# Kernel optimization log

Hardware: AMD Instinct MI355X
Metric: run time of the kernel (lower is better)

The kernel has to match this reference:

```python
import jax, jax.numpy as jnp
import numpy as np

B, Cin, H, W = 8, 128, 64, 64
Cout, K, S, P = 128, 3, 1, 1
KK = K * K


def _conv(x, w, b=None):
    y = jax.lax.conv_general_dilated(
        x, w, window_strides=(S, S), padding=[(P, P), (P, P)],
        dimension_numbers=("NCHW", "OIHW", "NCHW"))
    if b is not None:
        y = y + b[None, :, None, None]
    return y


def setup_inputs() -> dict:
    key = jax.random.key(0)
    ks = jax.random.split(key, 6)
    x = jax.random.normal(ks[0], (B, Cin, H, W), jnp.float32)
    # offset/modulator convs are zero-init in the module; use small random
    # values so learned-offset sampling path is actually exercised.
    w_off = jax.random.normal(ks[1], (2 * KK, Cin, K, K), jnp.float32) * 0.01
    b_off = jax.random.normal(ks[2], (2 * KK,), jnp.float32) * 0.1
    w_mod = jax.random.normal(ks[3], (KK, Cin, K, K), jnp.float32) * 0.01
    b_mod = jax.random.normal(ks[4], (KK,), jnp.float32) * 0.1
    w_reg = jax.random.normal(ks[5], (Cout, Cin, K, K), jnp.float32) * (1.0 / np.sqrt(Cin * KK))
    return {"x": x, "w_off": w_off, "b_off": b_off,
            "w_mod": w_mod, "b_mod": b_mod, "w_reg": w_reg}


def _deform_conv2d(x, offset, mask, w_reg):
    # offset: [B, 2*KK, Hout, Wout] with (dy, dx) interleaved per tap (torchvision layout)
    Hout, Wout = offset.shape[2], offset.shape[3]
    off = offset.reshape(B, KK, 2, Hout, Wout)
    dy = off[:, :, 0].transpose(0, 2, 3, 1)  # [B,Hout,Wout,KK]
    dx = off[:, :, 1].transpose(0, 2, 3, 1)
    kh = (jnp.arange(KK) // K).astype(jnp.float32)
    kw = (jnp.arange(KK) % K).astype(jnp.float32)
    ho = jnp.arange(Hout, dtype=jnp.float32) * S - P
    wo = jnp.arange(Wout, dtype=jnp.float32) * S - P
    py = ho[None, :, None, None] + kh[None, None, None, :] + dy  # [B,Hout,Wout,KK]
    px = wo[None, None, :, None] + kw[None, None, None, :] + dx
    y0f = jnp.floor(py); x0f = jnp.floor(px)
    wy = (py - y0f)[..., None]; wx = (px - x0f)[..., None]
    y0 = y0f.astype(jnp.int32); x0 = x0f.astype(jnp.int32)
    x_bhwc = x.transpose(0, 2, 3, 1)  # [B,H,W,Cin]
    bidx = jnp.arange(B).reshape(B, 1, 1, 1)

    def gather(yi, xi):
        valid = ((yi >= 0) & (yi < H) & (xi >= 0) & (xi < W)).astype(x.dtype)
        v = x_bhwc[bidx, jnp.clip(yi, 0, H - 1), jnp.clip(xi, 0, W - 1)]
        return v * valid[..., None]  # [B,Hout,Wout,KK,Cin], zero outside

    v00 = gather(y0, x0)
    v01 = gather(y0, x0 + 1)
    v10 = gather(y0 + 1, x0)
    v11 = gather(y0 + 1, x0 + 1)
    val = (v00 * (1 - wy) * (1 - wx) + v01 * (1 - wy) * wx
           + v10 * wy * (1 - wx) + v11 * wy * wx)
    # modulated deformable conv v2: mask [B,KK,Hout,Wout]
    val = val * mask.transpose(0, 2, 3, 1)[..., None]
    # weighted accumulation over taps and input channels -> NCHW output
    return jnp.einsum("bhwkc,ock->bohw", val, w_reg.reshape(Cout, Cin, KK))


def reference(x, w_off, b_off, w_mod, b_mod, w_reg):
    offset = _conv(x, w_off, b_off)
    mask = 2.0 * jax.nn.sigmoid(_conv(x, w_mod, b_mod))
    return _deform_conv2d(x, offset, mask, w_reg)
```

## Files before the change

### kernel.cpp

```cpp
#include <hip/hip_runtime.h>
#include <hip/hip_bf16.h>
#include <math.h>

#define H 64
#define W 64
#define CIN 128
#define COUT 128
#define BATCH 8
#define NPIX (H*W)
#define PXT 32
#define AP  136
#define RP  36
#define VSZ (PXT*AP)

typedef __attribute__((ext_vector_type(8))) short bf16x8;
typedef __attribute__((ext_vector_type(4))) float f32x4;
typedef __attribute__((ext_vector_type(16))) float f32x16;

static __device__ inline short f2bf(float f) {
  union { float f; unsigned u; } v; v.f = f;
  unsigned r = v.u + 0x7FFF + ((v.u >> 16) & 1);
  return (short)(r >> 16);
}
static __device__ inline float bf_lo(unsigned u) {
  union { unsigned u; float f; } v; v.u = u << 16; return v.f;
}
static __device__ inline float bf_hi(unsigned u) {
  union { unsigned u; float f; } v; v.u = u & 0xffff0000u; return v.f;
}

__global__ __launch_bounds__(256) void k_prep(const float* __restrict__ x,
    short* __restrict__ xbh,
    const float* __restrict__ w_off, const float* __restrict__ w_mod,
    short* __restrict__ wOMs, const float* __restrict__ w_reg,
    short* __restrict__ wAs) {
  __shared__ float tile[32][65];
  int blk = blockIdx.x;
  int t = threadIdx.x;
  if (blk < 2048) {
    int cg = blk & 3, y = (blk >> 2) & 63, b = blk >> 8;
#pragma unroll
    for (int j = 0; j < 2; ++j) {
      int f = t + j * 256;
      int ci = f >> 4, xi4 = f & 15;
      float4 v = *(const float4*)&x[(((b * CIN + cg * 32 + ci) * H + y) * W) + xi4 * 4];
      *(float4*)&tile[ci][xi4 * 4] = v;
    }
    __syncthreads();
#pragma unroll
    for (int i = 0; i < 2; ++i) {
      int idx = t + i * 256;
      int xi = idx >> 3, cig = idx & 7;
      float f0 = tile[cig * 4 + 0][xi];
      float f1 = tile[cig * 4 + 1][xi];
      float f2 = tile[cig * 4 + 2][xi];
      float f3 = tile[cig * 4 + 3][xi];
      __hip_bfloat162 h01 = __float22bfloat162_rn(make_float2(f0, f1));
      __hip_bfloat162 h23 = __float22bfloat162_rn(make_float2(f2, f3));
      uint2 pk;
      pk.x = *(unsigned*)&h01; pk.y = *(unsigned*)&h23;
      *(uint2*)&xbh[((b * H + y) * W + xi) * CIN + cg * 32 + cig * 4] = pk;
    }
  } else if (blk < 2048 + 144) {
    int e = (blk - 2048) * 256 + t;
    int tap = e >> 12, oc = (e >> 7) & 31, c = e & 127;
    float v = 0.f;
    if (oc < 18)      v = w_off[(oc * 128 + c) * 9 + tap];
    else if (oc < 27) v = w_mod[((oc - 18) * 128 + c) * 9 + tap];
    int kstep = c >> 4, g = (c >> 3) & 1, j = c & 7;
    int lane = g * 32 + oc;
    int o = ((tap * 8 + kstep) * 64 + lane) * 8 + j;
    wOMs[o] = f2bf(v);
  } else {
    int e = (blk - 2192) * 256 + t;
    int tap = e >> 14, oc = (e >> 7) & 127, c = e & 127;
    int kstep = c >> 4, g = (c >> 3) & 1, j = c & 7;
    int ms = oc >> 5, m = oc & 31;
    int lane = g * 32 + m;
    int o = (((tap * 8 + kstep) * 4 + ms) * 64 + lane) * 8 + j;
    wAs[o] = f2bf(w_reg[(oc * 128 + c) * 9 + tap]);
  }
}

__global__ __launch_bounds__(512, 8) void k_deform(const short* __restrict__ xbh,
    const short* __restrict__ wOMs, const float* __restrict__ b_off,
    const float* __restrict__ b_mod, const short* __restrict__ wAs,
    float* __restrict__ out) {
  __shared__ __align__(16) char smem_u[31104];
  __shared__ __align__(16) float  pw[PXT * 9 * 4];
  __shared__ __align__(16) ushort pa4[PXT * 9 * 4];
  float* red  = (float*)smem_u;
  short* vs   = (short*)smem_u;
  float* redE = (float*)smem_u;

  int blk = blockIdx.x;
  int b = blk & 7, tile = blk >> 3;
  int pix0 = tile * PXT;
  int t = threadIdx.x;
  int lane = t & 63;
  int wv = t >> 6;
  int n32 = lane & 31, g = lane >> 5;

  const short* xbB = xbh + (size_t)b * NPIX * CIN;

  {
    f32x16 accO = {};
#pragma unroll
    for (int ti = 0; ti < 2; ++ti) {
      int tap = wv + ti * 8;
      if (tap > 8) break;
      int dy = tap / 3 - 1, dx = tap % 3 - 1;
      int gp = pix0 + n32;
      int y = (gp >> 6) + dy, x = (gp & 63) + dx;
      int ok = ((unsigned)y < H) && ((unsigned)x < W);
      int lin = ok ? ((y << 6) + x) : 0;
#pragma unroll
      for (int kstep = 0; kstep < 8; ++kstep) {
        bf16x8 a = *(const bf16x8*)&wOMs[((tap * 8 + kstep) * 64 + lane) * 8];
        int c0 = kstep * 16 + g * 8;
        bf16x8 bv = *(const bf16x8*)&xbB[(size_t)lin * CIN + c0];
        if (!ok) bv = (bf16x8){};
        accO = __builtin_amdgcn_mfma_f32_32x32x16_bf16(a, bv, accO, 0, 0, 0);
      }
    }
#pragma unroll
    for (int r = 0; r < 16; ++r) {
      int row = (r & 3) + 8 * (r >> 2) + 4 * g;
      if (row < 27) red[wv * (27 * RP) + row * RP + n32] = accO[r];
    }
  }
  __syncthreads();

  for (int i = t; i < PXT * 9; i += 512) {
    int tap = i % 9, p = i / 9;
    float dyv = b_off[2 * tap], dxv = b_off[2 * tap + 1], z = b_mod[tap];
#pragma unroll
    for (int w = 0; w < 8; ++w) {
      const float* rw = red + w * (27 * RP);
      dyv += rw[(2 * tap) * RP + p];
      dxv += rw[(2 * tap + 1) * RP + p];
      z   += rw[(18 + tap) * RP + p];
    }
    float m = 2.f / (1.f + expf(-z));
    int gp = pix0 + p;
    float py = (float)((gp >> 6) - 1 + tap / 3) + dyv;
    float pxx = (float)((gp & 63) - 1 + tap % 3) + dxv;
    float yf = floorf(py), xf = floorf(pxx);
    float wy = py - yf, wx = pxx - xf;
    int y0 = (int)yf, x0 = (int)xf;
    int y1 = y0 + 1, x1 = x0 + 1;
    float vy0 = ((unsigned)y0 < H) ? 1.f : 0.f;
    float vy1 = ((unsigned)y1 < H) ? 1.f : 0.f;
    float vx0 = ((unsigned)x0 < W) ? 1.f : 0.f;
    float vx1 = ((unsigned)x1 < W) ? 1.f : 0.f;
    int y0c = min(max(y0, 0), H - 1), y1c = min(max(y1, 0), H - 1);
    int x0c = min(max(x0, 0), W - 1), x1c = min(max(x1, 0), W - 1);
    *(float4*)&pw[i * 4] = make_float4((1.f - wy) * (1.f - wx) * m * vy0 * vx0,
                                       (1.f - wy) * wx * m * vy0 * vx1,
                                       wy * (1.f - wx) * m * vy1 * vx0,
                                       wy * wx * m * vy1 * vx1);
    pa4[i * 4 + 0] = (ushort)((y0c << 6) + x0c);
    pa4[i * 4 + 1] = (ushort)((y0c << 6) + x1c);
    pa4[i * 4 + 2] = (ushort)((y1c << 6) + x0c);
    pa4[i * 4 + 3] = (ushort)((y1c << 6) + x1c);
  }
  __syncthreads();

  int ms = wv & 3, ks = wv >> 2;
  int cq = t & 15, ps = t >> 4;
  int c0s = cq * 8;

  f32x16 acc = {};

  for (int tap = 0; tap < 9; ++tap) {
    short* vbuf = vs + (tap & 1) * VSZ;

    {
      int idx = (ps * 9 + tap) * 4;
      float4 wq = *(const float4*)&pw[idx];
      uint4 u00 = *(const uint4*)&xbB[(int)pa4[idx]     * CIN + c0s];
      uint4 u01 = *(const uint4*)&xbB[(int)pa4[idx + 1] * CIN + c0s];
      uint4 u10 = *(const uint4*)&xbB[(int)pa4[idx + 2] * CIN + c0s];
      uint4 u11 = *(const uint4*)&xbB[(int)pa4[idx + 3] * CIN + c0s];
      uint4 packed;
#pragma unroll
      for (int j = 0; j < 4; ++j) {
        unsigned ua = ((const unsigned*)&u00)[j];
        unsigned ub = ((const unsigned*)&u01)[j];
        unsigned uc = ((const unsigned*)&u10)[j];
        unsigned ud = ((const unsigned*)&u11)[j];
        float s0 = fmaf(wq.w, bf_lo(ud), fmaf(wq.z, bf_lo(uc),
                   fmaf(wq.y, bf_lo(ub), wq.x * bf_lo(ua))));
        float s1 = fmaf(wq.w, bf_hi(ud), fmaf(wq.z, bf_hi(uc),
                   fmaf(wq.y, bf_hi(ub), wq.x * bf_hi(ua))));
        __hip_bfloat162 h2 = __float22bfloat162_rn(make_float2(s0, s1));
        ((unsigned*)&packed)[j] = *(unsigned*)&h2;
      }
      *(uint4*)&vbuf[ps * AP + c0s] = packed;
    }

    bf16x8 af[4];
#pragma unroll
    for (int i = 0; i < 4; ++i) {
      int kstep = ks * 4 + i;
      af[i] = *(const bf16x8*)&wAs[(((tap * 8 + kstep) * 4 + ms) * 64 + lane) * 8];
    }
    __syncthreads();

#pragma unroll
    for (int i = 0; i < 4; ++i) {
      int kstep = ks * 4 + i;
      int c0 = kstep * 16 + g * 8;
      bf16x8 bfr = *(const bf16x8*)&vbuf[n32 * AP + c0];
      acc = __builtin_amdgcn_mfma_f32_32x32x16_bf16(af[i], bfr, acc, 0, 0, 0);
    }
  }

  __syncthreads();
  if (ks == 1) {
#pragma unroll
    for (int r = 0; r < 16; ++r) {
      int row = (r & 3) + 8 * (r >> 2) + 4 * g;
      redE[ms * (32 * 33) + row * 33 + n32] = acc[r];
    }
  }
  __syncthreads();
  if (ks == 0) {
#pragma unroll
    for (int r = 0; r < 16; ++r) {
      int row = (r & 3) + 8 * (r >> 2) + 4 * g;
      float v = acc[r] + redE[ms * (32 * 33) + row * 33 + n32];
      out[(size_t)(b * COUT + ms * 32 + row) * NPIX + pix0 + n32] = v;
    }
  }
}

extern "C" void kernel_launch(void* const* d_in, const int* in_sizes, int n_in,
                              void* d_out, int out_size, void* d_ws, size_t ws_size,
                              hipStream_t stream) {
  const float* x     = (const float*)d_in[0];
  const float* w_off = (const float*)d_in[1];
  const float* b_off = (const float*)d_in[2];
  const float* w_mod = (const float*)d_in[3];
  const float* b_mod = (const float*)d_in[4];
  const float* w_reg = (const float*)d_in[5];

  short* xbh  = (short*)d_ws;
  short* wAs  = xbh + 4194304;
  short* wOMs = wAs + 147456;
  float* out  = (float*)d_out;

  k_prep<<<dim3(2768), 256, 0, stream>>>(x, xbh, w_off, w_mod, wOMs,
                                         w_reg, wAs);
  k_deform<<<dim3(NPIX / PXT * BATCH), 512, 0, stream>>>(
      xbh, wOMs, b_off, b_mod, wAs, out);
}
```

Before: 112.0 us.

## Balance offset-conv MFMA work across waves and split output reduction between halves

```diff
diff --git a/kernel.cpp b/kernel.cpp
--- a/kernel.cpp
+++ b/kernel.cpp
@@ -14,6 +14,7 @@
 #define VSZ (PXT*AP)
 
 typedef __attribute__((ext_vector_type(8))) short bf16x8;
+typedef __attribute__((ext_vector_type(2))) float f32x2;
 typedef __attribute__((ext_vector_type(4))) float f32x4;
 typedef __attribute__((ext_vector_type(16))) float f32x16;
 
@@ -22,11 +23,10 @@
   unsigned r = v.u + 0x7FFF + ((v.u >> 16) & 1);
   return (short)(r >> 16);
 }
-static __device__ inline float bf_lo(unsigned u) {
-  union { unsigned u; float f; } v; v.u = u << 16; return v.f;
-}
-static __device__ inline float bf_hi(unsigned u) {
-  union { unsigned u; float f; } v; v.u = u & 0xffff0000u; return v.f;
+static __device__ inline f32x2 bfpair(unsigned u) {
+  union { unsigned u; float f; } lo, hi;
+  lo.u = u << 16; hi.u = u & 0xffff0000u;
+  f32x2 r; r.x = lo.f; r.y = hi.f; return r;
 }
 
 __global__ __launch_bounds__(256) void k_prep(const float* __restrict__ x,
@@ -105,23 +105,28 @@
 
   {
     f32x16 accO = {};
-#pragma unroll
-    for (int ti = 0; ti < 2; ++ti) {
-      int tap = wv + ti * 8;
-      if (tap > 8) break;
-      int dy = tap / 3 - 1, dx = tap % 3 - 1;
-      int gp = pix0 + n32;
-      int y = (gp >> 6) + dy, x = (gp & 63) + dx;
-      int ok = ((unsigned)y < H) && ((unsigned)x < W);
-      int lin = ok ? ((y << 6) + x) : 0;
-#pragma unroll
-      for (int kstep = 0; kstep < 8; ++kstep) {
-        bf16x8 a = *(const bf16x8*)&wOMs[((tap * 8 + kstep) * 64 + lane) * 8];
-        int c0 = kstep * 16 + g * 8;
-        bf16x8 bv = *(const bf16x8*)&xbB[(size_t)lin * CIN + c0];
-        if (!ok) bv = (bf16x8){};
-        accO = __builtin_amdgcn_mfma_f32_32x32x16_bf16(a, bv, accO, 0, 0, 0);
-      }
+    int p0 = wv * 9;
+    int tapA = p0 >> 3, tapB = (p0 + 8) >> 3;
+    int gp = pix0 + n32;
+    int yb = gp >> 6, xb = gp & 63;
+    int yA = yb + tapA / 3 - 1, xA = xb + tapA % 3 - 1;
+    int yB = yb + tapB / 3 - 1, xB = xb + tapB % 3 - 1;
+    int okA = ((unsigned)yA < H) && ((unsigned)xA < W);
+    int okB = ((unsigned)yB < H) && ((unsigned)xB < W);
+    int linA = okA ? ((yA << 6) + xA) : 0;
+    int linB = okB ? ((yB << 6) + xB) : 0;
+#pragma unroll
+    for (int u = 0; u < 9; ++u) {
+      int pair = p0 + u;
+      int kstep = pair & 7;
+      int useB = (pair >> 3) != tapA;
+      int lin = useB ? linB : linA;
+      int ok  = useB ? okB  : okA;
+      bf16x8 a = *(const bf16x8*)&wOMs[(pair * 64 + lane) * 8];
+      int c0 = kstep * 16 + g * 8;
+      bf16x8 bv = *(const bf16x8*)&xbB[(size_t)lin * CIN + c0];
+      if (!ok) bv = (bf16x8){};
+      accO = __builtin_amdgcn_mfma_f32_32x32x16_bf16(a, bv, accO, 0, 0, 0);
     }
 #pragma unroll
     for (int r = 0; r < 16; ++r) {
@@ -141,7 +146,7 @@
       dxv += rw[(2 * tap + 1) * RP + p];
       z   += rw[(18 + tap) * RP + p];
     }
-    float m = 2.f / (1.f + expf(-z));
+    float m = 2.f / (1.f + __expf(-z));
     int gp = pix0 + p;
     float py = (float)((gp >> 6) - 1 + tap / 3) + dyv;
     float pxx = (float)((gp & 63) - 1 + tap % 3) + dxv;
@@ -185,15 +190,11 @@
       uint4 packed;
 #pragma unroll
       for (int j = 0; j < 4; ++j) {
-        unsigned ua = ((const unsigned*)&u00)[j];
-        unsigned ub = ((const unsigned*)&u01)[j];
-        unsigned uc = ((const unsigned*)&u10)[j];
-        unsigned ud = ((const unsigned*)&u11)[j];
-        float s0 = fmaf(wq.w, bf_lo(ud), fmaf(wq.z, bf_lo(uc),
-                   fmaf(wq.y, bf_lo(ub), wq.x * bf_lo(ua))));
-        float s1 = fmaf(wq.w, bf_hi(ud), fmaf(wq.z, bf_hi(uc),
-                   fmaf(wq.y, bf_hi(ub), wq.x * bf_hi(ua))));
-        __hip_bfloat162 h2 = __float22bfloat162_rn(make_float2(s0, s1));
+        f32x2 s = bfpair(((const unsigned*)&u00)[j]) * wq.x;
+        s += bfpair(((const unsigned*)&u01)[j]) * wq.y;
+        s += bfpair(((const unsigned*)&u10)[j]) * wq.z;
+        s += bfpair(((const unsigned*)&u11)[j]) * wq.w;
+        __hip_bfloat162 h2 = __float22bfloat162_rn(make_float2(s.x, s.y));
         ((unsigned*)&packed)[j] = *(unsigned*)&h2;
       }
       *(uint4*)&vbuf[ps * AP + c0s] = packed;
@@ -217,17 +218,17 @@
   }
 
   __syncthreads();
-  if (ks == 1) {
-#pragma unroll
-    for (int r = 0; r < 16; ++r) {
+#pragma unroll
+  for (int r = 0; r < 16; ++r) {
+    if ((r < 8) == (ks == 1)) {
       int row = (r & 3) + 8 * (r >> 2) + 4 * g;
       redE[ms * (32 * 33) + row * 33 + n32] = acc[r];
     }
   }
   __syncthreads();
-  if (ks == 0) {
-#pragma unroll
-    for (int r = 0; r < 16; ++r) {
+#pragma unroll
+  for (int r = 0; r < 16; ++r) {
+    if ((r < 8) == (ks == 0)) {
       int row = (r & 3) + 8 * (r >> 2) + 4 * g;
       float v = acc[r] + redE[ms * (32 * 33) + row * 33 + n32];
       out[(size_t)(b * COUT + ms * 32 + row) * NPIX + pix0 + n32] = v;
```

New measurement: 115.8 us. 1.03x slower.
